# Kernel optimization log

Measured on AMD Instinct MI355X. Metric: run time of the kernel, lower is better.

## Reference

```python
import jax, jax.numpy as jnp
import numpy as np

B, SEQ, D = 4, 4096, 64      # batch, sequence length, head dim
BS = 32                      # block_size_sparsity
V = 512                      # relative-info embedding vocabulary
R = SEQ // BS                # block rows per batch


def setup_inputs() -> dict:
    key = jax.random.key(0)
    k1, k2, k3 = jax.random.split(key, 3)
    q = jax.random.normal(k1, (B, SEQ, D), jnp.float32)
    emb = jax.random.normal(k2, (B, V, D), jnp.float32)
    # causal lower-triangular block-sparsity layout -> nonzero indices
    rb, cb = np.tril_indices(R)
    idxs_batch = jnp.asarray(np.repeat(np.arange(B), rb.size), jnp.int32)
    idxs_row = jnp.asarray(np.tile(rb, B), jnp.int32)
    P = B * rb.size  # number of nonzero sparse blocks (= 33024)
    info = jax.random.randint(k3, (P, BS, BS), 0, V, jnp.int32)
    return {"q": q, "emb": emb, "info": info,
            "idxs_batch": idxs_batch, "idxs_row": idxs_row}


def reference(q, emb, info, idxs_batch, idxs_row):
    # out[p,i,j] = <q[b_p, r_p*BS + i, :], emb[b_p, info[p,i,j], :]>
    # Compute dense per-batch scores once, then gather per sparse block.
    scores = jnp.einsum('bmd,bvd->bmv', q, emb)            # [B, SEQ, V]
    rows = idxs_row[:, None] * BS + jnp.arange(BS, dtype=jnp.int32)  # [P, BS]
    out = scores[idxs_batch[:, None, None], rows[:, :, None], info]  # [P, BS, BS]
    return out
```

## Files before the change

kernel.cpp:

```cpp
#include <hip/hip_runtime.h>

#define Bn   4
#define SEQn 4096
#define Dn   64
#define BSn  32
#define Vn   512
#define Rn   128
#define PPB  8256

#define TM   64
#define TVb  128
#define QP   68
#define EP   132

__global__ __launch_bounds__(256) void scores_kernel(
    const float* __restrict__ q, const float* __restrict__ emb,
    float* __restrict__ scores)
{
  __shared__ float sq[Dn * QP];
  __shared__ float se[Dn * EP];

  int bx   = blockIdx.x;
  int vblk = bx & 3;
  int bblk = (bx >> 2) & 3;
  int mblk = bx >> 4;
  int m0 = mblk * TM;
  int v0 = vblk * TVb;

  const float* qbase = q   + ((size_t)bblk * SEQn + m0) * Dn;
  const float* ebase = emb + ((size_t)bblk * Vn   + v0) * Dn;

  int t = threadIdx.x;
  for (int idx = t; idx < TM * Dn / 4; idx += 256) {
    int e = idx * 4;
    int m = e >> 6;
    int d = e & 63;
    float4 x = *(const float4*)(qbase + (size_t)m * Dn + d);
    sq[(d + 0) * QP + m] = x.x;
    sq[(d + 1) * QP + m] = x.y;
    sq[(d + 2) * QP + m] = x.z;
    sq[(d + 3) * QP + m] = x.w;
  }
  for (int idx = t; idx < TVb * Dn / 4; idx += 256) {
    int e = idx * 4;
    int v = e >> 6;
    int d = e & 63;
    float4 x = *(const float4*)(ebase + (size_t)v * Dn + d);
    se[(d + 0) * EP + v] = x.x;
    se[(d + 1) * EP + v] = x.y;
    se[(d + 2) * EP + v] = x.z;
    se[(d + 3) * EP + v] = x.w;
  }
  __syncthreads();

  int tx = t & 31;
  int ty = t >> 5;
  int ml = ty * 8;
  int vl = tx * 4;

  float acc[8][4];
#pragma unroll
  for (int r = 0; r < 8; ++r)
#pragma unroll
    for (int k = 0; k < 4; ++k) acc[r][k] = 0.0f;

#pragma unroll 4
  for (int d = 0; d < Dn; ++d) {
    float4 qa = *(const float4*)&sq[d * QP + ml];
    float4 qb = *(const float4*)&sq[d * QP + ml + 4];
    float4 ev = *(const float4*)&se[d * EP + vl];
    float qr[8] = {qa.x, qa.y, qa.z, qa.w, qb.x, qb.y, qb.z, qb.w};
    float ek[4] = {ev.x, ev.y, ev.z, ev.w};
#pragma unroll
    for (int r = 0; r < 8; ++r)
#pragma unroll
      for (int k = 0; k < 4; ++k) acc[r][k] += qr[r] * ek[k];
  }

  float* obase = scores + ((size_t)bblk * SEQn + m0) * Vn + v0;
#pragma unroll
  for (int r = 0; r < 8; ++r) {
    float4 st = {acc[r][0], acc[r][1], acc[r][2], acc[r][3]};
    *(float4*)(obase + (size_t)(ml + r) * Vn + vl) = st;
  }
}

#define GCHUNK 16

__global__ __launch_bounds__(512) void gather_kernel(
    const float* __restrict__ scores, const int* __restrict__ info,
    float* __restrict__ out)
{
  __shared__ float slab[BSn * Vn];

  int cid = blockIdx.x;
  int b   = blockIdx.y;

  int g = 0;
  while (8 * (g + 1) * (g + 2) <= cid) ++g;
  int local = cid - 8 * g * (g + 1);
  int rq    = local / (g + 1);
  int chunk = local - rq * (g + 1);
  int r     = 16 * g + rq;
  int np    = min(GCHUNK, (r + 1) - chunk * GCHUNK);
  size_t p0 = (size_t)b * PPB + ((size_t)r * (r + 1)) / 2 + (size_t)chunk * GCHUNK;

  int tid = threadIdx.x;
  int sub = tid >> 8;
  int t   = tid & 255;
  int rowoff = (t >> 3) << 9;

  const int4* info4 = (const int4*)info;
  float4*     out4  = (float4*)out;

  int4 iv[8];
#pragma unroll
  for (int k = 0; k < 8; ++k) {
    int pp = 2 * k + sub;
    size_t p = p0 + (pp < np ? pp : 0);
    iv[k] = info4[p * 256 + t];
  }

  {
    const float4* src = (const float4*)(scores + ((size_t)b * SEQn + (size_t)r * BSn) * Vn);
    float4* dst = (float4*)slab;
    for (int idx = tid; idx < BSn * Vn / 4; idx += 512) dst[idx] = src[idx];
  }
  __syncthreads();

#pragma unroll
  for (int k = 0; k < 8; ++k) {
    int pp = 2 * k + sub;
    if (pp < np) {
      float4 o;
      o.x = slab[rowoff + iv[k].x];
      o.y = slab[rowoff + iv[k].y];
      o.z = slab[rowoff + iv[k].z];
      o.w = slab[rowoff + iv[k].w];
      out4[(p0 + pp) * 256 + t] = o;
    }
  }
}

extern "C" void kernel_launch(void* const* d_in, const int* in_sizes, int n_in,
                              void* d_out, int out_size, void* d_ws, size_t ws_size,
                              hipStream_t stream) {
  const float* q    = (const float*)d_in[0];
  const float* emb  = (const float*)d_in[1];
  const int*   info = (const int*)d_in[2];

  float* scores = (float*)d_ws;
  float* out    = (float*)d_out;

  int gemm_blocks = (SEQn / TM) * Bn * (Vn / TVb);
  scores_kernel<<<gemm_blocks, 256, 0, stream>>>(q, emb, scores);

  dim3 ggrid(576, Bn);
  gather_kernel<<<ggrid, 512, 0, stream>>>(scores, info, out);
}
```

Baseline: 268.1 us.

## Restructure gather into persistent balanced row-pair blocks with double-buffered score slabs

The gather kernel now launches one 1024-thread block per (batch, row-pair). Each block handles rows k and 127-k, so every block has the same amount of causal work. Each block streams four 16-row halves of the score slab through two LDS buffers, loading the next half from global memory while the current one is gathered. Info indices are prefetched one iteration ahead in a strided loop. This removes the uneven chunked grid and overlaps slab loads with gathering. The cost is a small grid of 256 large blocks, each holding only one prefetched info load per thread, which may cut the number of memory requests in flight.

```diff
diff --git a/kernel.cpp b/kernel.cpp
--- a/kernel.cpp
+++ b/kernel.cpp
@@ -85,61 +85,76 @@
   }
 }
 
-#define GCHUNK 16
+#define HS (16 * Vn)
 
-__global__ __launch_bounds__(512) void gather_kernel(
+__device__ __forceinline__ void gather_half(
+    const float* __restrict__ buf, const int4* __restrict__ info4,
+    float4* __restrict__ out4, int b, int r, int h, int tid)
+{
+  int np = r + 1;
+  size_t p0 = (size_t)b * PPB + ((size_t)r * (r + 1)) / 2;
+  int pq = tid >> 7;
+  int l  = tid & 127;
+  int rowoff = (l >> 3) << 9;
+  int eo = 128 * h + l;
+
+  size_t pfirst = p0 + (pq < np ? pq : 0);
+  int4 iv = info4[pfirst * 256 + eo];
+  for (int pp = pq; pp < np; pp += 8) {
+    int4 cur = iv;
+    if (pp + 8 < np) iv = info4[(p0 + pp + 8) * 256 + eo];
+    float4 o;
+    o.x = buf[rowoff + cur.x];
+    o.y = buf[rowoff + cur.y];
+    o.z = buf[rowoff + cur.z];
+    o.w = buf[rowoff + cur.w];
+    out4[(p0 + pp) * 256 + eo] = o;
+  }
+}
+
+__global__ __launch_bounds__(1024) void gather_kernel(
     const float* __restrict__ scores, const int* __restrict__ info,
     float* __restrict__ out)
 {
-  __shared__ float slab[BSn * Vn];
+  __shared__ float bufA[HS];
+  __shared__ float bufB[HS];
 
-  int cid = blockIdx.x;
-  int b   = blockIdx.y;
-
-  int g = 0;
-  while (8 * (g + 1) * (g + 2) <= cid) ++g;
-  int local = cid - 8 * g * (g + 1);
-  int rq    = local / (g + 1);
-  int chunk = local - rq * (g + 1);
-  int r     = 16 * g + rq;
-  int np    = min(GCHUNK, (r + 1) - chunk * GCHUNK);
-  size_t p0 = (size_t)b * PPB + ((size_t)r * (r + 1)) / 2 + (size_t)chunk * GCHUNK;
-
+  int blk = blockIdx.x;
+  int b   = blk >> 6;
+  int k   = blk & 63;
+  int rA  = 127 - k;
+  int rB  = k;
   int tid = threadIdx.x;
-  int sub = tid >> 8;
-  int t   = tid & 255;
-  int rowoff = (t >> 3) << 9;
 
   const int4* info4 = (const int4*)info;
   float4*     out4  = (float4*)out;
 
-  int4 iv[8];
-#pragma unroll
-  for (int k = 0; k < 8; ++k) {
-    int pp = 2 * k + sub;
-    size_t p = p0 + (pp < np ? pp : 0);
-    iv[k] = info4[p * 256 + t];
-  }
+  const float4* s0 = (const float4*)(scores + ((size_t)b * SEQn + (size_t)rA * BSn +  0) * Vn);
+  const float4* s1 = (const float4*)(scores + ((size_t)b * SEQn + (size_t)rA * BSn + 16) * Vn);
+  const float4* s2 = (const float4*)(scores + ((size_t)b * SEQn + (size_t)rB * BSn +  0) * Vn);
+  const float4* s3 = (const float4*)(scores + ((size_t)b * SEQn + (size_t)rB * BSn + 16) * Vn);
 
-  {
-    const float4* src = (const float4*)(scores + ((size_t)b * SEQn + (size_t)r * BSn) * Vn);
-    float4* dst = (float4*)slab;
-    for (int idx = tid; idx < BSn * Vn / 4; idx += 512) dst[idx] = src[idx];
-  }
+  float4 r0, r1;
+
+  r0 = s0[tid]; r1 = s0[tid + 1024];
+  ((float4*)bufA)[tid] = r0; ((float4*)bufA)[tid + 1024] = r1;
+  r0 = s1[tid]; r1 = s1[tid + 1024];
   __syncthreads();
+  gather_half(bufA, info4, out4, b, rA, 0, tid);
 
-#pragma unroll
-  for (int k = 0; k < 8; ++k) {
-    int pp = 2 * k + sub;
-    if (pp < np) {
-      float4 o;
-      o.x = slab[rowoff + iv[k].x];
-      o.y = slab[rowoff + iv[k].y];
-      o.z = slab[rowoff + iv[k].z];
-      o.w = slab[rowoff + iv[k].w];
-      out4[(p0 + pp) * 256 + t] = o;
-    }
-  }
+  ((float4*)bufB)[tid] = r0; ((float4*)bufB)[tid + 1024] = r1;
+  r0 = s2[tid]; r1 = s2[tid + 1024];
+  __syncthreads();
+  gather_half(bufB, info4, out4, b, rA, 1, tid);
+
+  ((float4*)bufA)[tid] = r0; ((float4*)bufA)[tid + 1024] = r1;
+  r0 = s3[tid]; r1 = s3[tid + 1024];
+  __syncthreads();
+  gather_half(bufA, info4, out4, b, rB, 0, tid);
+
+  ((float4*)bufB)[tid] = r0; ((float4*)bufB)[tid + 1024] = r1;
+  __syncthreads();
+  gather_half(bufB, info4, out4, b, rB, 1, tid);
 }
 
 extern "C" void kernel_launch(void* const* d_in, const int* in_sizes, int n_in,
@@ -155,6 +170,5 @@
   int gemm_blocks = (SEQn / TM) * Bn * (Vn / TVb);
   scores_kernel<<<gemm_blocks, 256, 0, stream>>>(q, emb, scores);
 
-  dim3 ggrid(576, Bn);
-  gather_kernel<<<ggrid, 512, 0, stream>>>(scores, info, out);
+  gather_kernel<<<Bn * 64, 1024, 0, stream>>>(scores, info, out);
 }
```

New measurement: 287.4 us. +7.2%, slower.
